# Kernel optimization log

Measured on AMD Instinct MI355X. Metric: run time of the kernel, lower is better.

## Reference

```python
import jax, jax.numpy as jnp
import numpy as np

B, T, E = 4, 2048, 1024
H, D = 16, 64

def setup_inputs() -> dict:
    key = jax.random.key(0)
    k0, k1, k2, k3 = jax.random.split(key, 4)
    x = jax.random.normal(k0, (B, T, E), dtype=jnp.float32)
    Wq = jax.random.normal(k1, (H, E, D), dtype=jnp.float32) * (E ** -0.5)
    Wk = jax.random.normal(k2, (H, E, D), dtype=jnp.float32) * (E ** -0.5)
    Wv = jax.random.normal(k3, (H, E, D), dtype=jnp.float32) * (E ** -0.5)
    return {"x": x, "Wq": Wq, "Wk": Wk, "Wv": Wv}

def reference(x, Wq, Wk, Wv):
    # per-head projections: [B,T,E] x [H,E,D] -> [B,H,T,D]
    q = jnp.einsum('bte,hed->bhtd', x, Wq)
    k = jnp.einsum('bte,hed->bhtd', x, Wk)
    v = jnp.einsum('bte,hed->bhtd', x, Wv)
    d = q.shape[-1]
    scores = jnp.einsum('bhtd,bhsd->bhts', q, k) / jnp.sqrt(jnp.asarray(d, q.dtype))
    Tlen = x.shape[1]
    causal = jnp.tril(jnp.ones((Tlen, Tlen), dtype=bool))
    scores = jnp.where(causal, scores, -jnp.inf)
    weights = jax.nn.softmax(scores, axis=-1)
    out = jnp.einsum('bhts,bhsd->bhtd', weights, v)  # [B,H,T,D]
    # concat heads along last dim (head order preserved like torch.cat)
    Bb, Hh, Tt, Dd = out.shape
    return out.transpose(0, 2, 1, 3).reshape(Bb, Tt, Hh * Dd)
```

## Files before the change

### kernel.cpp

```cpp
#include <hip/hip_runtime.h>
#include <hip/hip_bf16.h>

#define BATCH 4
#define SEQ   2048
#define EMB   1024
#define NH    16
#define HD    64

#define Q_OFF  ((size_t)0)
#define K_OFF  ((size_t)8388608)
#define V_OFF  ((size_t)16777216)
#define WT_OFF ((size_t)25165824)

typedef __attribute__((ext_vector_type(8))) short short8;
typedef __attribute__((ext_vector_type(4))) short short4v;
typedef __attribute__((ext_vector_type(4))) float f32x4;
typedef __attribute__((ext_vector_type(4))) unsigned int uint4v;

__device__ __forceinline__ short8 pack8s(float4 a, float4 b, float s) {
    alignas(16) __hip_bfloat16 t[8] = {
        __float2bfloat16(a.x * s), __float2bfloat16(a.y * s),
        __float2bfloat16(a.z * s), __float2bfloat16(a.w * s),
        __float2bfloat16(b.x * s), __float2bfloat16(b.y * s),
        __float2bfloat16(b.z * s), __float2bfloat16(b.w * s)};
    return *reinterpret_cast<const short8*>(t);
}

__device__ __forceinline__ void async16(void* lds, const void* g) {
    __builtin_amdgcn_global_load_lds(
        (const __attribute__((address_space(1))) unsigned int*)g,
        (__attribute__((address_space(3))) unsigned int*)lds, 16, 0, 0);
}

__global__ __launch_bounds__(256)
void xcast_kernel(const float* __restrict__ x, __hip_bfloat16* __restrict__ xb)
{
    const size_t i = ((size_t)blockIdx.x * 256 + threadIdx.x) * 8;
    float4 f0 = ((const float4*)(x + i))[0];
    float4 f1 = ((const float4*)(x + i))[1];
    *(short8*)(xb + i) = pack8s(f0, f1, 1.0f);
}

__global__ __launch_bounds__(256)
void wt_kernel(const float* __restrict__ Wq, const float* __restrict__ Wk,
               const float* __restrict__ Wv, __hip_bfloat16* __restrict__ Wt)
{
    const int et = blockIdx.x;
    const int mh = blockIdx.y;
    const int m = mh >> 4, h = mh & 15;
    const float* W = ((m == 0) ? Wq : (m == 1) ? Wk : Wv) + (size_t)h * (EMB * HD);
    const float scale = (m == 0) ? 0.18033688011112042f : 1.0f;

    __shared__ __hip_bfloat16 T[64][72];
    const int tid = threadIdx.x;
    const int r   = tid >> 2;
    const int seg = (tid & 3) * 16;

    {
        const float* src = W + (size_t)(et * 64 + r) * HD + seg;
        float4 f0 = ((const float4*)src)[0];
        float4 f1 = ((const float4*)src)[1];
        float4 f2 = ((const float4*)src)[2];
        float4 f3 = ((const float4*)src)[3];
        const float v[16] = {f0.x,f0.y,f0.z,f0.w, f1.x,f1.y,f1.z,f1.w,
                             f2.x,f2.y,f2.z,f2.w, f3.x,f3.y,f3.z,f3.w};
        #pragma unroll
        for (int j = 0; j < 16; ++j) T[seg + j][r] = __float2bfloat16(v[j] * scale);
    }
    __syncthreads();
    __hip_bfloat16* dst = Wt + ((size_t)mh * HD + r) * EMB + et * 64 + seg;
    *(short8*)dst       = *(const short8*)&T[r][seg];
    *(short8*)(dst + 8) = *(const short8*)&T[r][seg + 8];
}

__global__ __launch_bounds__(256)
void qkv_proj_kernel(const __hip_bfloat16* __restrict__ xb,
                     const __hip_bfloat16* __restrict__ Wt,
                     __hip_bfloat16* __restrict__ qkv)
{
    const int nt = blockIdx.x;
    const int rt = blockIdx.y;
    const int row0 = rt * 128;
    const int n0   = nt * 128;

    __shared__ __hip_bfloat16 lds[17408];
    __hip_bfloat16* As = lds;
    __hip_bfloat16* Bs = lds + 8192;

    const int tid  = threadIdx.x;
    const int wave = tid >> 6;
    const int lane = tid & 63;
    const int lr   = lane & 15;
    const int lg   = lane >> 4;

    const int srow  = lane >> 3;
    const int sslot = (lane & 7) ^ srow;
    const char* aSrc = (const char*)xb + (size_t)(row0 + wave * 32 + srow) * 2048 + sslot * 16;
    const char* bSrc = (const char*)Wt + (size_t)(n0   + wave * 32 + srow) * 2048 + sslot * 16;
    char* aDst = (char*)As + (size_t)(wave * 32) * 128;
    char* bDst = (char*)Bs + (size_t)(wave * 32) * 128;

    f32x4 acc[2][8] = {};

    for (int k0 = 0; k0 < EMB; k0 += 64) {
        __syncthreads();
        #pragma unroll
        for (int i = 0; i < 4; ++i) {
            async16(aDst + i * 1024, aSrc + (size_t)i * 16384 + k0 * 2);
            async16(bDst + i * 1024, bSrc + (size_t)i * 16384 + k0 * 2);
        }
        __syncthreads();

        #pragma unroll
        for (int half = 0; half < 2; ++half) {
            const int cg = half * 4 + lg;
            const int r0a = wave * 32 + lr;
            const int r1a = wave * 32 + 16 + lr;
            short8 a0 = *(const short8*)((char*)As + r0a * 128 + ((cg ^ (r0a & 7)) * 16));
            short8 a1 = *(const short8*)((char*)As + r1a * 128 + ((cg ^ (r1a & 7)) * 16));
            #pragma unroll
            for (int ct = 0; ct < 8; ++ct) {
                const int rb = ct * 16 + lr;
                short8 bf = *(const short8*)((char*)Bs + rb * 128 + ((cg ^ (rb & 7)) * 16));
                acc[0][ct] = __builtin_amdgcn_mfma_f32_16x16x32_bf16(a0, bf, acc[0][ct], 0, 0, 0);
                acc[1][ct] = __builtin_amdgcn_mfma_f32_16x16x32_bf16(a1, bf, acc[1][ct], 0, 0, 0);
            }
        }
    }

    const int m = n0 >> 10;
    const int b = row0 >> 11;
    const int t0 = row0 & (SEQ - 1);
    __hip_bfloat16 (*Ts)[136] = (__hip_bfloat16(*)[136])lds;

    __syncthreads();
    if (m < 2) {
        #pragma unroll
        for (int rsub = 0; rsub < 2; ++rsub)
            #pragma unroll
            for (int ct = 0; ct < 8; ++ct)
                #pragma unroll
                for (int i = 0; i < 4; ++i)
                    Ts[wave * 32 + rsub * 16 + lg * 4 + i][ct * 16 + lr] =
                        __float2bfloat16(acc[rsub][ct][i]);
        __syncthreads();
        const int half = tid >> 7;
        const int t    = tid & 127;
        const int hq   = (2 * nt + half) & 15;
        __hip_bfloat16* hbase = qkv + ((m == 0) ? Q_OFF : K_OFF)
                              + (((size_t)b * NH + hq) * SEQ + t0) * HD;
        #pragma unroll
        for (int q = 0; q < 8; ++q) {
            const int c   = q * 128 + t;
            const int row = c >> 3;
            const int off = (c & 7) * 8;
            *(short8*)(hbase + (size_t)c * 8) = *(const short8*)&Ts[row][half * 64 + off];
        }
    } else {
        #pragma unroll
        for (int rsub = 0; rsub < 2; ++rsub)
            #pragma unroll
            for (int ct = 0; ct < 8; ++ct)
                #pragma unroll
                for (int i = 0; i < 4; ++i)
                    Ts[ct * 16 + lr][wave * 32 + rsub * 16 + lg * 4 + i] =
                        __float2bfloat16(acc[rsub][ct][i]);
        __syncthreads();
        const int l16 = tid & 15;
        #pragma unroll
        for (int q = 0; q < 8; ++q) {
            const int row = q * 16 + (tid >> 4);
            const int hv  = (2 * nt + (row >> 6)) & 15;
            const int dv  = row & 63;
            __hip_bfloat16* dst = qkv + V_OFF
                                + (((size_t)b * NH + hv) * HD + dv) * SEQ + t0 + l16 * 8;
            *(short8*)dst = *(const short8*)&Ts[row][l16 * 8];
        }
    }
}

__global__ __launch_bounds__(256)
void attn_kernel(const __hip_bfloat16* __restrict__ ws, float* __restrict__ out)
{
    const int bid = blockIdx.x;
    const int qt  = 15 - (bid >> 6);
    const int bh  = bid & 63;
    const int h   = bh & 15;
    const int b   = bh >> 4;
    const int qbase = qt * 128;
    const int ktmax = 2 * qt + 1;

    const __hip_bfloat16* qp = ws + Q_OFF + (size_t)bh * (SEQ * HD);
    const __hip_bfloat16* kp = ws + K_OFF + (size_t)bh * (SEQ * HD);
    const __hip_bfloat16* vt = ws + V_OFF + (size_t)bh * (HD * SEQ);

    __shared__ __align__(16) __hip_bfloat16 Ksb[2][4096];
    __shared__ __align__(16) __hip_bfloat16 Vsb[2][4096];

    const int tid  = threadIdx.x;
    const int wave = tid >> 6;
    const int lane = tid & 63;
    const int lr   = lane & 15;
    const int lg   = lane >> 4;
    const int l7   = lr & 7;

    const int srow8 = lane >> 3;
    const int sslot = (lane & 7) ^ srow8;

    short8 qf[2][2];
    #pragma unroll
    for (int rsub = 0; rsub < 2; ++rsub) {
        const __hip_bfloat16* src =
            qp + (size_t)(qbase + wave * 32 + rsub * 16 + lr) * HD + lg * 8;
        qf[rsub][0] = *(const short8*)src;
        qf[rsub][1] = *(const short8*)(src + 32);
    }

    float l_run[2] = {0.f, 0.f};
    f32x4 o_acc[2][4] = {};

    auto stage = [&](int buf, int kbase) {
        #pragma unroll
        for (int j = 0; j < 2; ++j) {
            const int r0 = wave * 16 + j * 8;
            async16((char*)Ksb[buf] + r0 * 128,
                    (const char*)(kp + (size_t)(kbase + r0 + srow8) * HD) + sslot * 16);
            async16((char*)Vsb[buf] + r0 * 128,
                    (const char*)(vt + (size_t)(r0 + srow8) * SEQ + kbase) + sslot * 16);
        }
    };

    stage(0, 0);
    __syncthreads();

    for (int kt = 0; kt <= ktmax; ++kt) {
        const int cur = kt & 1;
        if (kt < ktmax) stage(cur ^ 1, (kt + 1) * 64);

        f32x4 s[2][4];
        __builtin_amdgcn_s_setprio(1);
        #pragma unroll
        for (int ct = 0; ct < 4; ++ct) {
            const char* kb = (const char*)Ksb[cur] + (ct * 16 + lr) * 128;
            short8 kf0 = *(const short8*)(kb + ((lg      ^ l7) << 4));
            short8 kf1 = *(const short8*)(kb + (((lg + 4) ^ l7) << 4));
            #pragma unroll
            for (int rsub = 0; rsub < 2; ++rsub) {
                f32x4 z = {};
                z           = __builtin_amdgcn_mfma_f32_16x16x32_bf16(kf0, qf[rsub][0], z, 0, 0, 0);
                s[rsub][ct] = __builtin_amdgcn_mfma_f32_16x16x32_bf16(kf1, qf[rsub][1], z, 0, 0, 0);
            }
        }
        __builtin_amdgcn_s_setprio(0);

        const int kbase = kt * 64;
        if (kt >= 2 * qt) {
            #pragma unroll
            for (int rsub = 0; rsub < 2; ++rsub) {
                const int qrow = qbase + wave * 32 + rsub * 16 + lr;
                #pragma unroll
                for (int ct = 0; ct < 4; ++ct)
                    #pragma unroll
                    for (int i = 0; i < 4; ++i) {
                        const int key = kbase + ct * 16 + lg * 4 + i;
                        s[rsub][ct][i] = (key > qrow) ? -1e30f : s[rsub][ct][i];
                    }
            }
        }

        short8 pf[2][2];
        #pragma unroll
        for (int rsub = 0; rsub < 2; ++rsub) {
            unsigned int Wp[4][2];
            float rs0 = 0.f, rs1 = 0.f;
            #pragma unroll
            for (int ct = 0; ct < 4; ++ct) {
                const float p0 = __builtin_amdgcn_exp2f(s[rsub][ct][0]);
                const float p1 = __builtin_amdgcn_exp2f(s[rsub][ct][1]);
                const float p2 = __builtin_amdgcn_exp2f(s[rsub][ct][2]);
                const float p3 = __builtin_amdgcn_exp2f(s[rsub][ct][3]);
                rs0 += p0 + p1;
                rs1 += p2 + p3;
                asm("v_cvt_pk_bf16_f32 %0, %1, %2" : "=v"(Wp[ct][0]) : "v"(p0), "v"(p1));
                asm("v_cvt_pk_bf16_f32 %0, %1, %2" : "=v"(Wp[ct][1]) : "v"(p2), "v"(p3));
            }
            l_run[rsub] += rs0 + rs1;

            unsigned int d0[4], d1[4];
            #pragma unroll
            for (int w = 0; w < 2; ++w) {
                unsigned int A = Wp[0][w], B = Wp[1][w];
                asm volatile("v_permlane32_swap_b32 %0, %1" : "+v"(A), "+v"(B));
                asm volatile("v_permlane16_swap_b32 %0, %1" : "+v"(A), "+v"(B));
                d0[w] = A; d0[2 + w] = B;
                unsigned int C = Wp[2][w], D = Wp[3][w];
                asm volatile("v_permlane32_swap_b32 %0, %1" : "+v"(C), "+v"(D));
                asm volatile("v_permlane16_swap_b32 %0, %1" : "+v"(C), "+v"(D));
                d1[w] = C; d1[2 + w] = D;
            }
            uint4v t0 = {d0[0], d0[1], d0[2], d0[3]};
            uint4v t1 = {d1[0], d1[1], d1[2], d1[3]};
            pf[rsub][0] = __builtin_bit_cast(short8, t0);
            pf[rsub][1] = __builtin_bit_cast(short8, t1);
        }

        __builtin_amdgcn_s_setprio(1);
        #pragma unroll
        for (int ct = 0; ct < 4; ++ct) {
            const char* vb = (const char*)Vsb[cur] + (ct * 16 + lr) * 128;
            short8 vf0 = *(const short8*)(vb + ((lg      ^ l7) << 4));
            short8 vf1 = *(const short8*)(vb + (((lg + 4) ^ l7) << 4));
            #pragma unroll
            for (int rsub = 0; rsub < 2; ++rsub) {
                o_acc[rsub][ct] = __builtin_amdgcn_mfma_f32_16x16x32_bf16(vf0, pf[rsub][0], o_acc[rsub][ct], 0, 0, 0);
                o_acc[rsub][ct] = __builtin_amdgcn_mfma_f32_16x16x32_bf16(vf1, pf[rsub][1], o_acc[rsub][ct], 0, 0, 0);
            }
        }
        __builtin_amdgcn_s_setprio(0);

        __syncthreads();
    }

    float* op = out + (size_t)b * SEQ * (NH * HD) + (size_t)h * HD;
    #pragma unroll
    for (int rsub = 0; rsub < 2; ++rsub) {
        float l = l_run[rsub];
        l += __shfl_xor(l, 16, 64);
        l += __shfl_xor(l, 32, 64);
        const float inv  = 1.0f / l;
        const int   trow = qbase + wave * 32 + rsub * 16 + lr;
        #pragma unroll
        for (int ct = 0; ct < 4; ++ct) {
            float4 o;
            o.x = o_acc[rsub][ct][0] * inv;
            o.y = o_acc[rsub][ct][1] * inv;
            o.z = o_acc[rsub][ct][2] * inv;
            o.w = o_acc[rsub][ct][3] * inv;
            *(float4*)&op[(size_t)trow * (NH * HD) + ct * 16 + lg * 4] = o;
        }
    }
}

extern "C" void kernel_launch(void* const* d_in, const int* in_sizes, int n_in,
                              void* d_out, int out_size, void* d_ws, size_t ws_size,
                              hipStream_t stream) {
    const float* x  = (const float*)d_in[0];
    const float* Wq = (const float*)d_in[1];
    const float* Wk = (const float*)d_in[2];
    const float* Wv = (const float*)d_in[3];
    float* out = (float*)d_out;
    __hip_bfloat16* ws = (__hip_bfloat16*)d_ws;

    __hip_bfloat16* xb = (__hip_bfloat16*)d_out;

    hipLaunchKernelGGL(xcast_kernel, dim3((BATCH * SEQ * EMB) / (256 * 8)), dim3(256),
                       0, stream, x, xb);
    hipLaunchKernelGGL(wt_kernel, dim3(16, 48), dim3(256), 0, stream,
                       Wq, Wk, Wv, ws + WT_OFF);
    hipLaunchKernelGGL(qkv_proj_kernel, dim3(24, 64), dim3(256), 0, stream,
                       xb, ws + WT_OFF, ws);
    hipLaunchKernelGGL(attn_kernel, dim3(1024), dim3(256), 0, stream, ws, out);
}
```

Measured before the change: 133.2 us.

## Pair causal query tiles per block and stage 128-key chunks for balanced attention

The attention kernel now launches 512 blocks, and each block handles two query tiles, p and 15-p, so every block does roughly the same causal work. The block index is remapped so neighbouring blocks spread across XCDs. K/V staging is widened to 128-key chunks, split into two 64-key halves, which halves the number of barriers per tile and doubles LDS use to 64KB. The cost is a serialised second segment per block and fewer resident blocks, which could lower occupancy or latency hiding.

```diff
diff --git a/kernel.cpp b/kernel.cpp
--- a/kernel.cpp
+++ b/kernel.cpp
@@ -182,20 +182,19 @@
 __global__ __launch_bounds__(256)
 void attn_kernel(const __hip_bfloat16* __restrict__ ws, float* __restrict__ out)
 {
-    const int bid = blockIdx.x;
-    const int qt  = 15 - (bid >> 6);
-    const int bh  = bid & 63;
-    const int h   = bh & 15;
-    const int b   = bh >> 4;
-    const int qbase = qt * 128;
-    const int ktmax = 2 * qt + 1;
+    const int bid     = blockIdx.x;
+    const int logical = (bid & 7) * 64 + (bid >> 3);
+    const int p  = logical & 7;
+    const int bh = logical >> 3;
+    const int h  = bh & 15;
+    const int b  = bh >> 4;
 
     const __hip_bfloat16* qp = ws + Q_OFF + (size_t)bh * (SEQ * HD);
     const __hip_bfloat16* kp = ws + K_OFF + (size_t)bh * (SEQ * HD);
     const __hip_bfloat16* vt = ws + V_OFF + (size_t)bh * (HD * SEQ);
 
-    __shared__ __align__(16) __hip_bfloat16 Ksb[2][4096];
-    __shared__ __align__(16) __hip_bfloat16 Vsb[2][4096];
+    __shared__ __align__(16) __hip_bfloat16 Ksb[2][2][4096];
+    __shared__ __align__(16) __hip_bfloat16 Vsb[2][2][4096];
 
     const int tid  = threadIdx.x;
     const int wave = tid >> 6;
@@ -207,136 +206,147 @@
     const int srow8 = lane >> 3;
     const int sslot = (lane & 7) ^ srow8;
 
-    short8 qf[2][2];
-    #pragma unroll
-    for (int rsub = 0; rsub < 2; ++rsub) {
-        const __hip_bfloat16* src =
-            qp + (size_t)(qbase + wave * 32 + rsub * 16 + lr) * HD + lg * 8;
-        qf[rsub][0] = *(const short8*)src;
-        qf[rsub][1] = *(const short8*)(src + 32);
-    }
-
-    float l_run[2] = {0.f, 0.f};
-    f32x4 o_acc[2][4] = {};
-
-    auto stage = [&](int buf, int kbase) {
-        #pragma unroll
-        for (int j = 0; j < 2; ++j) {
-            const int r0 = wave * 16 + j * 8;
-            async16((char*)Ksb[buf] + r0 * 128,
-                    (const char*)(kp + (size_t)(kbase + r0 + srow8) * HD) + sslot * 16);
-            async16((char*)Vsb[buf] + r0 * 128,
-                    (const char*)(vt + (size_t)(r0 + srow8) * SEQ + kbase) + sslot * 16);
-        }
+    float* op = out + (size_t)b * SEQ * (NH * HD) + (size_t)h * HD;
+
+    auto stage = [&](int buf, int kb128) {
+        #pragma unroll
+        for (int hh = 0; hh < 2; ++hh)
+            #pragma unroll
+            for (int j = 0; j < 2; ++j) {
+                const int r0 = wave * 16 + j * 8;
+                async16((char*)Ksb[buf][hh] + r0 * 128,
+                        (const char*)(kp + (size_t)(kb128 + hh * 64 + r0 + srow8) * HD) + sslot * 16);
+                async16((char*)Vsb[buf][hh] + r0 * 128,
+                        (const char*)(vt + (size_t)(r0 + srow8) * SEQ + kb128 + hh * 64) + sslot * 16);
+            }
     };
 
-    stage(0, 0);
-    __syncthreads();
-
-    for (int kt = 0; kt <= ktmax; ++kt) {
-        const int cur = kt & 1;
-        if (kt < ktmax) stage(cur ^ 1, (kt + 1) * 64);
-
-        f32x4 s[2][4];
-        __builtin_amdgcn_s_setprio(1);
-        #pragma unroll
-        for (int ct = 0; ct < 4; ++ct) {
-            const char* kb = (const char*)Ksb[cur] + (ct * 16 + lr) * 128;
-            short8 kf0 = *(const short8*)(kb + ((lg      ^ l7) << 4));
-            short8 kf1 = *(const short8*)(kb + (((lg + 4) ^ l7) << 4));
-            #pragma unroll
-            for (int rsub = 0; rsub < 2; ++rsub) {
-                f32x4 z = {};
-                z           = __builtin_amdgcn_mfma_f32_16x16x32_bf16(kf0, qf[rsub][0], z, 0, 0, 0);
-                s[rsub][ct] = __builtin_amdgcn_mfma_f32_16x16x32_bf16(kf1, qf[rsub][1], z, 0, 0, 0);
+    for (int seg = 0; seg < 2; ++seg) {
+        const int qt    = seg ? (15 - p) : p;
+        const int qbase = qt * 128;
+
+        short8 qf[2][2];
+        #pragma unroll
+        for (int rsub = 0; rsub < 2; ++rsub) {
+            const __hip_bfloat16* src =
+                qp + (size_t)(qbase + wave * 32 + rsub * 16 + lr) * HD + lg * 8;
+            qf[rsub][0] = *(const short8*)src;
+            qf[rsub][1] = *(const short8*)(src + 32);
+        }
+
+        float l_run[2] = {0.f, 0.f};
+        f32x4 o_acc[2][4] = {};
+
+        stage(0, 0);
+        __syncthreads();
+
+        for (int kt = 0; kt <= qt; ++kt) {
+            const int cur = kt & 1;
+            if (kt < qt) stage(cur ^ 1, (kt + 1) * 128);
+
+            #pragma unroll
+            for (int hh = 0; hh < 2; ++hh) {
+                f32x4 s[2][4];
+                __builtin_amdgcn_s_setprio(1);
+                #pragma unroll
+                for (int ct = 0; ct < 4; ++ct) {
+                    const char* kb = (const char*)Ksb[cur][hh] + (ct * 16 + lr) * 128;
+                    short8 kf0 = *(const short8*)(kb + ((lg      ^ l7) << 4));
+                    short8 kf1 = *(const short8*)(kb + (((lg + 4) ^ l7) << 4));
+                    #pragma unroll
+                    for (int rsub = 0; rsub < 2; ++rsub) {
+                        f32x4 z = {};
+                        z           = __builtin_amdgcn_mfma_f32_16x16x32_bf16(kf0, qf[rsub][0], z, 0, 0, 0);
+                        s[rsub][ct] = __builtin_amdgcn_mfma_f32_16x16x32_bf16(kf1, qf[rsub][1], z, 0, 0, 0);
+                    }
+                }
+                __builtin_amdgcn_s_setprio(0);
+
+                if (kt == qt) {
+                    const int kbase = kt * 128 + hh * 64;
+                    #pragma unroll
+                    for (int rsub = 0; rsub < 2; ++rsub) {
+                        const int qrow = qbase + wave * 32 + rsub * 16 + lr;
+                        #pragma unroll
+                        for (int ct = 0; ct < 4; ++ct)
+                            #pragma unroll
+                            for (int i = 0; i < 4; ++i) {
+                                const int key = kbase + ct * 16 + lg * 4 + i;
+                                s[rsub][ct][i] = (key > qrow) ? -1e30f : s[rsub][ct][i];
+                            }
+                    }
+                }
+
+                short8 pf[2][2];
+                #pragma unroll
+                for (int rsub = 0; rsub < 2; ++rsub) {
+                    unsigned int Wp[4][2];
+                    float rs0 = 0.f, rs1 = 0.f;
+                    #pragma unroll
+                    for (int ct = 0; ct < 4; ++ct) {
+                        const float p0 = __builtin_amdgcn_exp2f(s[rsub][ct][0]);
+                        const float p1 = __builtin_amdgcn_exp2f(s[rsub][ct][1]);
+                        const float p2 = __builtin_amdgcn_exp2f(s[rsub][ct][2]);
+                        const float p3 = __builtin_amdgcn_exp2f(s[rsub][ct][3]);
+                        rs0 += p0 + p1;
+                        rs1 += p2 + p3;
+                        asm("v_cvt_pk_bf16_f32 %0, %1, %2" : "=v"(Wp[ct][0]) : "v"(p0), "v"(p1));
+                        asm("v_cvt_pk_bf16_f32 %0, %1, %2" : "=v"(Wp[ct][1]) : "v"(p2), "v"(p3));
+                    }
+                    l_run[rsub] += rs0 + rs1;
+
+                    unsigned int d0[4], d1[4];
+                    #pragma unroll
+                    for (int w = 0; w < 2; ++w) {
+                        unsigned int A = Wp[0][w], B = Wp[1][w];
+                        asm volatile("v_permlane32_swap_b32 %0, %1" : "+v"(A), "+v"(B));
+                        asm volatile("v_permlane16_swap_b32 %0, %1" : "+v"(A), "+v"(B));
+                        d0[w] = A; d0[2 + w] = B;
+                        unsigned int C = Wp[2][w], D = Wp[3][w];
+                        asm volatile("v_permlane32_swap_b32 %0, %1" : "+v"(C), "+v"(D));
+                        asm volatile("v_permlane16_swap_b32 %0, %1" : "+v"(C), "+v"(D));
+                        d1[w] = C; d1[2 + w] = D;
+                    }
+                    uint4v t0 = {d0[0], d0[1], d0[2], d0[3]};
+                    uint4v t1 = {d1[0], d1[1], d1[2], d1[3]};
+                    pf[rsub][0] = __builtin_bit_cast(short8, t0);
+                    pf[rsub][1] = __builtin_bit_cast(short8, t1);
+                }
+
+                __builtin_amdgcn_s_setprio(1);
+                #pragma unroll
+                for (int ct = 0; ct < 4; ++ct) {
+                    const char* vb = (const char*)Vsb[cur][hh] + (ct * 16 + lr) * 128;
+                    short8 vf0 = *(const short8*)(vb + ((lg      ^ l7) << 4));
+                    short8 vf1 = *(const short8*)(vb + (((lg + 4) ^ l7) << 4));
+                    #pragma unroll
+                    for (int rsub = 0; rsub < 2; ++rsub) {
+                        o_acc[rsub][ct] = __builtin_amdgcn_mfma_f32_16x16x32_bf16(vf0, pf[rsub][0], o_acc[rsub][ct], 0, 0, 0);
+                        o_acc[rsub][ct] = __builtin_amdgcn_mfma_f32_16x16x32_bf16(vf1, pf[rsub][1], o_acc[rsub][ct], 0, 0, 0);
+                    }
+                }
+                __builtin_amdgcn_s_setprio(0);
             }
-        }
-        __builtin_amdgcn_s_setprio(0);
-
-        const int kbase = kt * 64;
-        if (kt >= 2 * qt) {
-            #pragma unroll
-            for (int rsub = 0; rsub < 2; ++rsub) {
-                const int qrow = qbase + wave * 32 + rsub * 16 + lr;
-                #pragma unroll
-                for (int ct = 0; ct < 4; ++ct)
-                    #pragma unroll
-                    for (int i = 0; i < 4; ++i) {
-                        const int key = kbase + ct * 16 + lg * 4 + i;
-                        s[rsub][ct][i] = (key > qrow) ? -1e30f : s[rsub][ct][i];
-                    }
+
+            __syncthreads();
+        }
+
+        #pragma unroll
+        for (int rsub = 0; rsub < 2; ++rsub) {
+            float l = l_run[rsub];
+            l += __shfl_xor(l, 16, 64);
+            l += __shfl_xor(l, 32, 64);
+            const float inv  = 1.0f / l;
+            const int   trow = qbase + wave * 32 + rsub * 16 + lr;
+            #pragma unroll
+            for (int ct = 0; ct < 4; ++ct) {
+                float4 o;
+                o.x = o_acc[rsub][ct][0] * inv;
+                o.y = o_acc[rsub][ct][1] * inv;
+                o.z = o_acc[rsub][ct][2] * inv;
+                o.w = o_acc[rsub][ct][3] * inv;
+                *(float4*)&op[(size_t)trow * (NH * HD) + ct * 16 + lg * 4] = o;
             }
-        }
-
-        short8 pf[2][2];
-        #pragma unroll
-        for (int rsub = 0; rsub < 2; ++rsub) {
-            unsigned int Wp[4][2];
-            float rs0 = 0.f, rs1 = 0.f;
-            #pragma unroll
-            for (int ct = 0; ct < 4; ++ct) {
-                const float p0 = __builtin_amdgcn_exp2f(s[rsub][ct][0]);
-                const float p1 = __builtin_amdgcn_exp2f(s[rsub][ct][1]);
-                const float p2 = __builtin_amdgcn_exp2f(s[rsub][ct][2]);
-                const float p3 = __builtin_amdgcn_exp2f(s[rsub][ct][3]);
-                rs0 += p0 + p1;
-                rs1 += p2 + p3;
-                asm("v_cvt_pk_bf16_f32 %0, %1, %2" : "=v"(Wp[ct][0]) : "v"(p0), "v"(p1));
-                asm("v_cvt_pk_bf16_f32 %0, %1, %2" : "=v"(Wp[ct][1]) : "v"(p2), "v"(p3));
-            }
-            l_run[rsub] += rs0 + rs1;
-
-            unsigned int d0[4], d1[4];
-            #pragma unroll
-            for (int w = 0; w < 2; ++w) {
-                unsigned int A = Wp[0][w], B = Wp[1][w];
-                asm volatile("v_permlane32_swap_b32 %0, %1" : "+v"(A), "+v"(B));
-                asm volatile("v_permlane16_swap_b32 %0, %1" : "+v"(A), "+v"(B));
-                d0[w] = A; d0[2 + w] = B;
-                unsigned int C = Wp[2][w], D = Wp[3][w];
-                asm volatile("v_permlane32_swap_b32 %0, %1" : "+v"(C), "+v"(D));
-                asm volatile("v_permlane16_swap_b32 %0, %1" : "+v"(C), "+v"(D));
-                d1[w] = C; d1[2 + w] = D;
-            }
-            uint4v t0 = {d0[0], d0[1], d0[2], d0[3]};
-            uint4v t1 = {d1[0], d1[1], d1[2], d1[3]};
-            pf[rsub][0] = __builtin_bit_cast(short8, t0);
-            pf[rsub][1] = __builtin_bit_cast(short8, t1);
-        }
-
-        __builtin_amdgcn_s_setprio(1);
-        #pragma unroll
-        for (int ct = 0; ct < 4; ++ct) {
-            const char* vb = (const char*)Vsb[cur] + (ct * 16 + lr) * 128;
-            short8 vf0 = *(const short8*)(vb + ((lg      ^ l7) << 4));
-            short8 vf1 = *(const short8*)(vb + (((lg + 4) ^ l7) << 4));
-            #pragma unroll
-            for (int rsub = 0; rsub < 2; ++rsub) {
-                o_acc[rsub][ct] = __builtin_amdgcn_mfma_f32_16x16x32_bf16(vf0, pf[rsub][0], o_acc[rsub][ct], 0, 0, 0);
-                o_acc[rsub][ct] = __builtin_amdgcn_mfma_f32_16x16x32_bf16(vf1, pf[rsub][1], o_acc[rsub][ct], 0, 0, 0);
-            }
-        }
-        __builtin_amdgcn_s_setprio(0);
-
-        __syncthreads();
-    }
-
-    float* op = out + (size_t)b * SEQ * (NH * HD) + (size_t)h * HD;
-    #pragma unroll
-    for (int rsub = 0; rsub < 2; ++rsub) {
-        float l = l_run[rsub];
-        l += __shfl_xor(l, 16, 64);
-        l += __shfl_xor(l, 32, 64);
-        const float inv  = 1.0f / l;
-        const int   trow = qbase + wave * 32 + rsub * 16 + lr;
-        #pragma unroll
-        for (int ct = 0; ct < 4; ++ct) {
-            float4 o;
-            o.x = o_acc[rsub][ct][0] * inv;
-            o.y = o_acc[rsub][ct][1] * inv;
-            o.z = o_acc[rsub][ct][2] * inv;
-            o.w = o_acc[rsub][ct][3] * inv;
-            *(float4*)&op[(size_t)trow * (NH * HD) + ct * 16 + lg * 4] = o;
         }
     }
 }
@@ -359,5 +369,5 @@
                        Wq, Wk, Wv, ws + WT_OFF);
     hipLaunchKernelGGL(qkv_proj_kernel, dim3(24, 64), dim3(256), 0, stream,
                        xb, ws + WT_OFF, ws);
-    hipLaunchKernelGGL(attn_kernel, dim3(1024), dim3(256), 0, stream, ws, out);
-}
+    hipLaunchKernelGGL(attn_kernel, dim3(512), dim3(256), 0, stream, ws, out);
+}
```

New measurement: 146.9 us. +10.3%, slower.
